# Kernel tuning notes

Measured on AMD Instinct MI355X. Metric: run time of the kernel, lower is better.

Reference implementation:

```python
import jax, jax.numpy as jnp
import numpy as np

K_NB = 16
HID = 64
CIN = 128
EPS = 1e-5


def knn_idx(q, t, k):
    # q [B,N,3] queries, t [B,M,3] targets -> idx [B,N,k] into targets
    d = (jnp.sum(q * q, -1)[:, :, None] + jnp.sum(t * t, -1)[:, None, :]
         - 2.0 * jnp.einsum('bnd,bmd->bnm', q, t))
    _, idx = jax.lax.top_k(-d, k)
    return idx


def gather(feat, idx):
    # feat [B,C,M], idx [B,N,K] -> [B,C,N,K]
    return jax.vmap(lambda f, i: f[:, i])(feat, idx)


def conv1x1(x, W, b):
    # x [B,C,N,K], W [O,C], b [O]
    return jnp.einsum('oc,bcnk->bonk', W, x) + b[None, :, None, None]


def group_norm(x, gamma, beta, groups):
    B, C, N, K = x.shape
    xg = x.reshape(B, groups, C // groups, N, K)
    m = xg.mean(axis=(2, 3, 4), keepdims=True)
    v = xg.var(axis=(2, 3, 4), keepdims=True)
    xg = (xg - m) / jnp.sqrt(v + EPS)
    x = xg.reshape(B, C, N, K)
    return x * gamma[None, :, None, None] + beta[None, :, None, None]


def leaky(x):
    return jnp.where(x >= 0, x, 0.1 * x)


def setup_inputs() -> dict:
    key = jax.random.key(0)
    ks = jax.random.split(key, 20)
    B, N = 2, 4096
    d = {
        'xyz0': jax.random.normal(ks[0], (B, 3, N), jnp.float32),
        'xyz1': jax.random.normal(ks[1], (B, 3, N), jnp.float32),
        'state': jax.random.normal(ks[2], (B, HID, N), jnp.float32),
        'corr0': jax.random.normal(ks[3], (B, HID, N), jnp.float32),
        'feat0': jax.random.normal(ks[4], (B, CIN, N), jnp.float32),
        'feat1': jax.random.normal(ks[5], (B, CIN, N), jnp.float32),
        'flow0': jax.random.normal(ks[6], (B, 3, N), jnp.float32),
        # flow_layer: SetConv(3, [64,64]) -> convs take 3+3=6 then 64 in-chans
        'fw1': jax.random.normal(ks[7], (64, 6), jnp.float32) * 0.05,
        'fb1': jnp.zeros((64,), jnp.float32),
        'fg1': jnp.ones((64,), jnp.float32),
        'fbe1': jnp.zeros((64,), jnp.float32),
        'fw2': jax.random.normal(ks[8], (64, 64), jnp.float32) * 0.05,
        'fb2': jnp.zeros((64,), jnp.float32),
        'fg2': jnp.ones((64,), jnp.float32),
        'fbe2': jnp.zeros((64,), jnp.float32),
        # GRU gates: SetConv in_feat = hid(64)+(hid+64=128)=192, +3 = 195 -> 64, no act
        'wz': jax.random.normal(ks[9], (HID, 195), jnp.float32) * 0.05,
        'bz': jnp.zeros((HID,), jnp.float32),
        'wr': jax.random.normal(ks[10], (HID, 195), jnp.float32) * 0.05,
        'br': jnp.zeros((HID,), jnp.float32),
        'wq': jax.random.normal(ks[11], (HID, 195), jnp.float32) * 0.05,
        'bq': jnp.zeros((HID,), jnp.float32),
        # interp weight_net: 2*128+3=259 -> 128 -> 64
        'wa1': jax.random.normal(ks[12], (CIN, 2 * CIN + 3), jnp.float32) * 0.05,
        'ba1': jnp.zeros((CIN,), jnp.float32),
        'wa2': jax.random.normal(ks[13], (HID, CIN), jnp.float32) * 0.05,
        'ba2': jnp.zeros((HID,), jnp.float32),
    }
    return d


def reference(xyz0, xyz1, state, corr0, feat0, feat1, flow0,
              fw1, fb1, fg1, fbe1, fw2, fb2, fg2, fbe2,
              wz, bz, wr, br, wq, bq, wa1, ba1, wa2, ba2):
    xyz0_t = xyz0.transpose(0, 2, 1)  # [B,N,3]
    xyz1_t = xyz1.transpose(0, 2, 1)

    # ---- flow_layer: SetConv (KNN, N==npoint so new_xyz = xyz0) ----
    idx0 = knn_idx(xyz0_t, xyz0_t, K_NB)              # [B,N,K]
    gxyz0 = gather(xyz0, idx0) - xyz0[:, :, :, None]  # [B,3,N,K]
    h = jnp.concatenate([gather(flow0, idx0), gxyz0], axis=1)  # [B,6,N,K]
    h = leaky(group_norm(conv1x1(h, fw1, fb1), fg1, fbe1, 64 // 16))
    h = leaky(group_norm(conv1x1(h, fw2, fb2), fg2, fbe2, 64 // 16))
    flow_feat = h.max(axis=3)  # [B,64,N]

    # ---- iter_layer: SetGRU over xyz0 neighbors ----
    feat_g = jnp.concatenate([corr0, flow_feat], axis=1)  # [B,128,N]

    def gate(f, W, b):
        g = jnp.concatenate([gather(f, idx0), gxyz0], axis=1)
        return conv1x1(g, W, b).max(axis=3)  # [B,64,N]

    hid_in = jnp.concatenate([feat_g, state], axis=1)  # [B,192,N]
    z = jax.nn.sigmoid(gate(hid_in, wz, bz))
    r = jax.nn.sigmoid(gate(hid_in, wr, br))
    q = jnp.tanh(gate(jnp.concatenate([feat_g, r * state], axis=1), wq, bq))
    next_state = (1.0 - z) * state + z * q  # [B,64,N]

    # ---- align_layer: SetInterp (queries xyz1, targets xyz0) ----
    idx1 = knn_idx(xyz1_t, xyz0_t, K_NB)
    gv = gather(next_state, idx1)                        # [B,64,N,K]
    gx = gather(xyz0, idx1) - xyz1[:, :, :, None]        # [B,3,N,K]
    gf = jnp.concatenate([
        gather(feat0, idx1),
        jnp.broadcast_to(feat1[:, :, :, None], feat1.shape + (K_NB,))], axis=1)
    w = conv1x1(jnp.concatenate([gf, gx], axis=1), wa1, ba1)
    w = conv1x1(leaky(w), wa2, ba2)
    w = jax.nn.softmax(w, axis=3)
    return jnp.sum(gv * w, axis=3)  # [B,64,N]
```

## Files before the change

kernel.cpp:

```cpp
#include <hip/hip_runtime.h>

#define B_SZ 2

__device__ __forceinline__ int rfl(int x) { return __builtin_amdgcn_readfirstlane(x); }
__device__ __forceinline__ float leaky(float v) { return v >= 0.f ? v : 0.1f * v; }

__launch_bounds__(256)
__global__ void pack_kernel(const float* __restrict__ xyz, float4* __restrict__ out, int N)
{
  int b = blockIdx.y;
  int i = blockIdx.x * 256 + threadIdx.x;
  if (i >= N) return;
  const float* p = xyz + (size_t)b * 3 * N;
  float x = p[i], y = p[N + i], z = p[2 * N + i];
  out[(size_t)b * N + i] = make_float4(x, y, z, x * x + y * y + z * z);
}

__launch_bounds__(256)
__global__ void knn_wave_kernel(const float4* __restrict__ pk, const float* __restrict__ q,
                                int* __restrict__ idx, int N)
{
  __shared__ float sx[1024], sy[1024], sz[1024], sw[1024];
  int b = blockIdx.y;
  int lane = threadIdx.x & 63, wav = rfl(threadIdx.x >> 6);
  int qi = blockIdx.x * 4 + wav;
  const float* qb = q + (size_t)b * 3 * N;
  float qx = qb[qi], qy = qb[N + qi], qz = qb[2 * N + qi];
  float qq = qx * qx + qy * qy + qz * qz;
  float bd = 3.0e38f;
  int   bi = 0;
  float thr = 3.0e38f;
  const float4* pb = pk + (size_t)b * N;
  for (int ch = 0; ch < N; ch += 1024) {
    __syncthreads();
    for (int i = threadIdx.x; i < 1024; i += 256) {
      float4 v = pb[ch + i];
      sx[i] = v.x; sy[i] = v.y; sz[i] = v.z; sw[i] = v.w;
    }
    __syncthreads();
    for (int sub = 0; sub < 1024; sub += 64) {
      int c = sub + lane;
      float dl = (qq + sw[c]) - 2.0f * (qx * sx[c] + qy * sy[c] + qz * sz[c]);
      unsigned long long qm = __ballot(dl < thr);
      while (qm) {
        int l = __ffsll(qm) - 1;
        qm &= qm - 1;
        float dc = __shfl(dl, l);
        unsigned long long rm = __ballot(lane < 16 && bd <= dc);
        int pos = __popcll(rm);
        if (pos < 16) {
          int ic = ch + sub + l;
          float pbd = __shfl(bd, lane - 1);
          int   pbi = __shfl(bi, lane - 1);
          if (lane < 16) {
            if (lane == pos)      { bd = dc;  bi = ic; }
            else if (lane > pos)  { bd = pbd; bi = pbi; }
          }
          thr = __shfl(bd, 15);
        }
      }
    }
  }
  if (lane < 16) idx[((size_t)b * N + qi) * 16 + lane] = bi;
}

__launch_bounds__(256)
__global__ void prep_w_kernel(const float* __restrict__ wz, const float* __restrict__ wr,
    const float* __restrict__ wq, const float* __restrict__ wa1,
    const float* __restrict__ bz, const float* __restrict__ br,
    float* __restrict__ WtZR, float* __restrict__ WtQ,
    float* __restrict__ WtU, float* __restrict__ WtV, float* __restrict__ bZR)
{
  int job = blockIdx.x;
  int tid = threadIdx.x;
  if (job == 0) {
    for (int e = tid; e < 195 * 128; e += 256) {
      int k = e >> 7, o = e & 127;
      const float* w = (o < 64) ? wz : wr;
      WtZR[(size_t)k * 128 + o] = w[(size_t)(o & 63) * 195 + k];
    }
    if (tid < 128) bZR[tid] = (tid < 64) ? bz[tid] : br[tid - 64];
  } else if (job == 1) {
    for (int e = tid; e < 195 * 64; e += 256) {
      int k = e >> 6, o = e & 63;
      WtQ[(size_t)k * 64 + o] = wq[(size_t)o * 195 + k];
    }
  } else if (job == 2) {
    for (int e = tid; e < 131 * 128; e += 256) {
      int k = e >> 7, o = e & 127;
      int col = (k < 128) ? k : 256 + (k - 128);
      WtU[(size_t)k * 128 + o] = wa1[(size_t)o * 259 + col];
    }
  } else {
    for (int e = tid; e < 131 * 128; e += 256) {
      int k = e >> 7, o = e & 127;
      float v = (k < 128) ? wa1[(size_t)o * 259 + 128 + k]
                          : -wa1[(size_t)o * 259 + 256 + (k - 128)];
      WtV[(size_t)k * 128 + o] = v;
    }
  }
}

#define KC 66
__launch_bounds__(256)
__global__ void projT_kernel(const float* __restrict__ Wt, int K, int WOUT,
    const float* __restrict__ bias, float* __restrict__ out,
    int N, int PN,
    const float* __restrict__ s0, int c0, int l0,
    const float* __restrict__ s1, int c1, int l1,
    const float* __restrict__ s2, int c2, int l2,
    const float* __restrict__ s3, int c3, int l3)
{
  __shared__ __align__(16) float Ws[KC][68];
  __shared__ __align__(16) float Xs[KC][68];
  const int n0 = blockIdx.x * 64;
  const int oo = blockIdx.y * 64;
  const int b = n0 / N;
  const int nn0 = n0 - b * N;
  const int tid = threadIdx.x;
  const int tx = tid & 15, ty = tid >> 4;
  const int o4 = tx * 4, n4 = ty * 4;
  float acc[4][4];
#pragma unroll
  for (int i = 0; i < 4; ++i)
#pragma unroll
    for (int j = 0; j < 4; ++j)
      acc[i][j] = bias ? bias[oo + o4 + j] : 0.0f;

  const int e01 = c0 + c1, e012 = c0 + c1 + c2;
  for (int k0 = 0; k0 < K; k0 += KC) {
    const int kc = min(KC, K - k0);
    __syncthreads();
    for (int e = tid; e < kc * 64; e += 256) {
      int k = e >> 6, o = e & 63;
      Ws[k][o] = Wt[(size_t)(k0 + k) * WOUT + oo + o];
    }
    for (int e = tid; e < kc * 64; e += 256) {
      int k = e >> 6, j = e & 63;
      int c = k0 + k;
      float v;
      if (c < c0)        v = l0 ? s0[(size_t)c * PN + n0 + j]
                                : s0[((size_t)b * c0 + c) * N + nn0 + j];
      else if (c < e01)  { int cc = c - c0;
                           v = l1 ? s1[(size_t)cc * PN + n0 + j]
                                  : s1[((size_t)b * c1 + cc) * N + nn0 + j]; }
      else if (c < e012) { int cc = c - e01;
                           v = l2 ? s2[(size_t)cc * PN + n0 + j]
                                  : s2[((size_t)b * c2 + cc) * N + nn0 + j]; }
      else               { int cc = c - e012;
                           v = l3 ? s3[(size_t)cc * PN + n0 + j]
                                  : s3[((size_t)b * c3 + cc) * N + nn0 + j]; }
      Xs[k][j] = v;
    }
    __syncthreads();
#pragma unroll 2
    for (int k = 0; k < kc; ++k) {
      float4 wv = *(const float4*)&Ws[k][o4];
      float4 xv = *(const float4*)&Xs[k][n4];
      acc[0][0] = fmaf(xv.x, wv.x, acc[0][0]); acc[0][1] = fmaf(xv.x, wv.y, acc[0][1]);
      acc[0][2] = fmaf(xv.x, wv.z, acc[0][2]); acc[0][3] = fmaf(xv.x, wv.w, acc[0][3]);
      acc[1][0] = fmaf(xv.y, wv.x, acc[1][0]); acc[1][1] = fmaf(xv.y, wv.y, acc[1][1]);
      acc[1][2] = fmaf(xv.y, wv.z, acc[1][2]); acc[1][3] = fmaf(xv.y, wv.w, acc[1][3]);
      acc[2][0] = fmaf(xv.z, wv.x, acc[2][0]); acc[2][1] = fmaf(xv.z, wv.y, acc[2][1]);
      acc[2][2] = fmaf(xv.z, wv.z, acc[2][2]); acc[2][3] = fmaf(xv.z, wv.w, acc[2][3]);
      acc[3][0] = fmaf(xv.w, wv.x, acc[3][0]); acc[3][1] = fmaf(xv.w, wv.y, acc[3][1]);
      acc[3][2] = fmaf(xv.w, wv.z, acc[3][2]); acc[3][3] = fmaf(xv.w, wv.w, acc[3][3]);
    }
  }
#pragma unroll
  for (int i = 0; i < 4; ++i) {
    float4 r = make_float4(acc[i][0], acc[i][1], acc[i][2], acc[i][3]);
    *(float4*)&out[(size_t)(n0 + n4 + i) * WOUT + oo + o4] = r;
  }
}

__device__ __forceinline__ void seg_accumL(const float* __restrict__ p, int cnt,
    const float* __restrict__ WL, int sC, int sN, long n0, float acc[4])
{
#pragma unroll 4
  for (int c = 0; c < cnt; ++c) {
    float w = WL[c];
    const float* pp = p + (size_t)c * sC + (size_t)n0 * sN;
#pragma unroll
    for (int m = 0; m < 4; ++m)
      acc[m] = fmaf(w, pp[(size_t)m * sN], acc[m]);
  }
}

template<int WP>
__launch_bounds__(256)
__global__ void proj_kernel(
    const float* __restrict__ W0, const float* __restrict__ bias,
    float* __restrict__ out, int OUTS, int wld, int N,
    const float* __restrict__ s0, int c0, int w0,
    const float* __restrict__ s1, int c1, int w1)
{
  __shared__ float Wl[64 * WP];
  const int b = blockIdx.y;
  const int lane = threadIdx.x & 63;
  const int wav = rfl(threadIdx.x >> 6);
  int lco = 0;
  for (int r = wav; r < 64; r += 4)
    for (int c = lane; c < c0; c += 64)
      Wl[r * WP + c] = W0[(size_t)r * wld + w0 + c];
  lco = c0;
  for (int r = wav; r < 64; r += 4)
    for (int c = lane; c < c1; c += 64)
      Wl[r * WP + lco + c] = W0[(size_t)r * wld + w1 + c];
  __syncthreads();
  const long n0 = ((long)blockIdx.x * 4 + wav) * 4;
  float bv = bias ? bias[lane] : 0.0f;
  float acc[4] = {bv, bv, bv, bv};
  const float* WL = &Wl[lane * WP];
  seg_accumL(s0 + (size_t)b * c0 * N, c0, WL, N, 1, n0, acc);
  seg_accumL(s1 + (size_t)b * c1 * N, c1, WL + c0, N, 1, n0, acc);
#pragma unroll
  for (int m = 0; m < 4; ++m)
    out[((size_t)b * N + n0 + m) * OUTS + lane] = acc[m];
}

__launch_bounds__(256)
__global__ void gn1_stats_kernel(const float* __restrict__ G1, const float* __restrict__ xyz0,
    const float* __restrict__ fw1, const int* __restrict__ idx0,
    float* __restrict__ stats1, int N)
{
  __shared__ float red[4][4][2];
  int b = blockIdx.y;
  int lane = threadIdx.x & 63, wav = rfl(threadIdx.x >> 6);
  float wg0 = fw1[lane * 6 + 3], wg1 = fw1[lane * 6 + 4], wg2 = fw1[lane * 6 + 5];
  const float* xb = xyz0 + (size_t)b * 3 * N;
  float sum = 0.f, sq = 0.f;
  for (int n = blockIdx.x * 4 + wav; n < N; n += gridDim.x * 4) {
    const int* ip = idx0 + ((size_t)b * N + n) * 16;
    float bx = wg0 * xb[n] + wg1 * xb[N + n] + wg2 * xb[2 * N + n];
#pragma unroll
    for (int k = 0; k < 16; ++k) {
      int m = ip[k];
      float y = G1[((size_t)b * N + m) * 64 + lane] - bx;
      sum += y; sq += y * y;
    }
  }
#pragma unroll
  for (int off = 1; off < 16; off <<= 1) {
    sum += __shfl_xor(sum, off, 64);
    sq += __shfl_xor(sq, off, 64);
  }
  int g = lane >> 4;
  if ((lane & 15) == 0) { red[wav][g][0] = sum; red[wav][g][1] = sq; }
  __syncthreads();
  if (threadIdx.x < 8) {
    int gg = threadIdx.x >> 1, s = threadIdx.x & 1;
    float v = red[0][gg][s] + red[1][gg][s] + red[2][gg][s] + red[3][gg][s];
    atomicAdd(&stats1[(b * 4 + gg) * 2 + s], v);
  }
}

__global__ void gn_finalize_kernel(const float* __restrict__ raw, float* __restrict__ mi, float cnt)
{
  int i = threadIdx.x;
  if (i < 8) {
    float s = raw[i * 2], q = raw[i * 2 + 1];
    float m = s / cnt;
    float v = q / cnt - m * m;
    mi[i * 2] = m;
    mi[i * 2 + 1] = rsqrtf(v + 1e-5f);
  }
}

__launch_bounds__(256, 2)
__global__ void conv2_kernel(const float* __restrict__ G1, const float* __restrict__ xyz0,
    const float* __restrict__ fw1, const int* __restrict__ idx0,
    const float* __restrict__ fw2, const float* __restrict__ fb2,
    const float* __restrict__ fg1, const float* __restrict__ fbe1,
    const float* __restrict__ mi1, float* __restrict__ y2max, float* __restrict__ y2min,
    float* __restrict__ stats2, int N)
{
  __shared__ __align__(16) float x2[4][16][64];
  __shared__ float red[4][4][2];
  const int b = blockIdx.y;
  const int lane = threadIdx.x & 63;
  const int wav = rfl(threadIdx.x >> 6);
  float4 w[16];
#pragma unroll
  for (int i = 0; i < 16; ++i) w[i] = *(const float4*)&fw2[lane * 64 + i * 4];
  float wg0 = fw1[lane * 6 + 3], wg1 = fw1[lane * 6 + 4], wg2 = fw1[lane * 6 + 5];
  const int g = lane >> 4;
  float mu1 = mi1[(b * 4 + g) * 2], inv1 = mi1[(b * 4 + g) * 2 + 1];
  float sc1 = fg1[lane] * inv1;
  float sh1 = fbe1[lane] - mu1 * sc1;
  float fb2l = fb2[lane];
  const float* xb = xyz0 + (size_t)b * 3 * N;
  float sum = 0.f, sq = 0.f;
  for (int n = blockIdx.x * 4 + wav; n < N; n += gridDim.x * 4) {
    const int* ip = idx0 + ((size_t)b * N + n) * 16;
    float bx = wg0 * xb[n] + wg1 * xb[N + n] + wg2 * xb[2 * N + n];
#pragma unroll
    for (int k = 0; k < 16; ++k) {
      int m = ip[k];
      float y = G1[((size_t)b * N + m) * 64 + lane] - bx;
      x2[wav][k][lane] = leaky(y * sc1 + sh1);
    }
    float acc[16];
#pragma unroll
    for (int k = 0; k < 16; ++k) acc[k] = fb2l;
#pragma unroll
    for (int c4 = 0; c4 < 16; ++c4) {
      float4 w4 = w[c4];
#pragma unroll
      for (int k = 0; k < 16; ++k) {
        float4 x4 = *(const float4*)&x2[wav][k][c4 * 4];
        acc[k] = fmaf(w4.x, x4.x, acc[k]);
        acc[k] = fmaf(w4.y, x4.y, acc[k]);
        acc[k] = fmaf(w4.z, x4.z, acc[k]);
        acc[k] = fmaf(w4.w, x4.w, acc[k]);
      }
    }
    float mx = -3.0e38f, mn = 3.0e38f;
#pragma unroll
    for (int k = 0; k < 16; ++k) {
      mx = fmaxf(mx, acc[k]); mn = fminf(mn, acc[k]);
      sum += acc[k]; sq += acc[k] * acc[k];
    }
    y2max[((size_t)b * N + n) * 64 + lane] = mx;
    y2min[((size_t)b * N + n) * 64 + lane] = mn;
  }
#pragma unroll
  for (int off = 1; off < 16; off <<= 1) {
    sum += __shfl_xor(sum, off, 64);
    sq += __shfl_xor(sq, off, 64);
  }
  if ((lane & 15) == 0) { red[wav][g][0] = sum; red[wav][g][1] = sq; }
  __syncthreads();
  if (threadIdx.x < 8) {
    int gg = threadIdx.x >> 1, s = threadIdx.x & 1;
    float v = red[0][gg][s] + red[1][gg][s] + red[2][gg][s] + red[3][gg][s];
    atomicAdd(&stats2[(b * 4 + gg) * 2 + s], v);
  }
}

__launch_bounds__(256)
__global__ void flow_feat_kernel(const float* __restrict__ y2max, const float* __restrict__ y2min,
    const float* __restrict__ mi2, const float* __restrict__ fg2, const float* __restrict__ fbe2,
    float* __restrict__ ff_t, int N, int PN)
{
  size_t i = (size_t)blockIdx.x * blockDim.x + threadIdx.x;
  if (i >= (size_t)B_SZ * N * 64) return;
  int c = i & 63;
  size_t pn = i >> 6;
  int b = (int)(pn / N);
  int g = c >> 4;
  float mu = mi2[(b * 4 + g) * 2], inv = mi2[(b * 4 + g) * 2 + 1];
  float sc = fg2[c] * inv;
  float sh = fbe2[c] - mu * sc;
  float y = (sc >= 0.0f) ? y2max[i] : y2min[i];
  ff_t[(size_t)c * PN + pn] = leaky(y * sc + sh);
}

__launch_bounds__(256)
__global__ void gate_zr_kernel(const float* __restrict__ Szr,
    const float* __restrict__ wz, const float* __restrict__ wr,
    const float* __restrict__ xyz0, const float* __restrict__ state,
    const int* __restrict__ idx0,
    float* __restrict__ zo, float* __restrict__ rs_t, int N, int PN)
{
  int b = blockIdx.y;
  int lane = threadIdx.x & 63, wav = rfl(threadIdx.x >> 6);
  float wz0 = wz[lane * 195 + 192], wz1 = wz[lane * 195 + 193], wz2 = wz[lane * 195 + 194];
  float wr0 = wr[lane * 195 + 192], wr1 = wr[lane * 195 + 193], wr2 = wr[lane * 195 + 194];
  const float* xb = xyz0 + (size_t)b * 3 * N;
  for (int n = blockIdx.x * 4 + wav; n < N; n += gridDim.x * 4) {
    const int* ip = idx0 + ((size_t)b * N + n) * 16;
    float u0 = xb[n], u1 = xb[N + n], u2 = xb[2 * N + n];
    float xz = wz0 * u0 + wz1 * u1 + wz2 * u2;
    float xr = wr0 * u0 + wr1 * u1 + wr2 * u2;
    float mz = -3.0e38f, mr = -3.0e38f;
#pragma unroll
    for (int k = 0; k < 16; ++k) {
      size_t mo = ((size_t)b * N + ip[k]) * 128 + lane;
      mz = fmaxf(mz, Szr[mo]);
      mr = fmaxf(mr, Szr[mo + 64]);
    }
    size_t no = ((size_t)b * N + n) * 64 + lane;
    float z = 1.f / (1.f + expf(-(mz - xz)));
    float r = 1.f / (1.f + expf(-(mr - xr)));
    zo[no] = z;
    rs_t[(size_t)lane * PN + (size_t)b * N + n] = r * state[((size_t)b * 64 + lane) * N + n];
  }
}

__launch_bounds__(256)
__global__ void gate_q_ns_kernel(const float* __restrict__ Sq, const float* __restrict__ wq,
    const float* __restrict__ xyz0, const float* __restrict__ zo,
    const float* __restrict__ state, const int* __restrict__ idx0,
    float* __restrict__ ns, int N)
{
  int b = blockIdx.y;
  int lane = threadIdx.x & 63, wav = rfl(threadIdx.x >> 6);
  float wq0 = wq[lane * 195 + 192], wq1 = wq[lane * 195 + 193], wq2 = wq[lane * 195 + 194];
  const float* xb = xyz0 + (size_t)b * 3 * N;
  for (int n = blockIdx.x * 4 + wav; n < N; n += gridDim.x * 4) {
    const int* ip = idx0 + ((size_t)b * N + n) * 16;
    float xq = wq0 * xb[n] + wq1 * xb[N + n] + wq2 * xb[2 * N + n];
    float mq = -3.0e38f;
#pragma unroll
    for (int k = 0; k < 16; ++k)
      mq = fmaxf(mq, Sq[((size_t)b * N + ip[k]) * 64 + lane]);
    size_t no = ((size_t)b * N + n) * 64 + lane;
    float q = tanhf(mq - xq);
    float z = zo[no];
    float st = state[((size_t)b * 64 + lane) * N + n];
    ns[no] = (1.f - z) * st + z * q;
  }
}

__launch_bounds__(256, 2)
__global__ void align_kernel(const float* __restrict__ U, const float* __restrict__ V,
    const float* __restrict__ wa2, const float* __restrict__ ba2,
    const float* __restrict__ ns, const int* __restrict__ idx1,
    float* __restrict__ out, int N)
{
  __shared__ __align__(16) float xk[4][16][128];
  const int b = blockIdx.y;
  const int lane = threadIdx.x & 63;
  const int wav = rfl(threadIdx.x >> 6);
  float4 w[32];
#pragma unroll
  for (int i = 0; i < 32; ++i) w[i] = *(const float4*)&wa2[lane * 128 + i * 4];
  float ba = ba2[lane];
  const int n = blockIdx.x * 4 + wav;
  const int* ip = idx1 + ((size_t)b * N + n) * 16;
  int mk[16];
#pragma unroll
  for (int k = 0; k < 16; ++k) mk[k] = ip[k];
  const float* Vp = V + ((size_t)b * N + n) * 128;
  float v0 = Vp[lane], v1 = Vp[64 + lane];
#pragma unroll
  for (int k = 0; k < 16; ++k) {
    const float* Up = U + ((size_t)b * N + mk[k]) * 128;
    xk[wav][k][lane] = leaky(Up[lane] + v0);
    xk[wav][k][64 + lane] = leaky(Up[64 + lane] + v1);
  }
  float acc[16];
#pragma unroll
  for (int k = 0; k < 16; ++k) acc[k] = ba;
#pragma unroll
  for (int c4 = 0; c4 < 32; ++c4) {
    float4 w4 = w[c4];
#pragma unroll
    for (int k = 0; k < 16; ++k) {
      float4 x4 = *(const float4*)&xk[wav][k][c4 * 4];
      acc[k] = fmaf(w4.x, x4.x, acc[k]);
      acc[k] = fmaf(w4.y, x4.y, acc[k]);
      acc[k] = fmaf(w4.z, x4.z, acc[k]);
      acc[k] = fmaf(w4.w, x4.w, acc[k]);
    }
  }
  float m = acc[0];
#pragma unroll
  for (int k = 1; k < 16; ++k) m = fmaxf(m, acc[k]);
  float s = 0.f;
#pragma unroll
  for (int k = 0; k < 16; ++k) { acc[k] = expf(acc[k] - m); s += acc[k]; }
  float rinv = 1.0f / s;
  float o = 0.f;
#pragma unroll
  for (int k = 0; k < 16; ++k)
    o += acc[k] * rinv * ns[((size_t)b * N + mk[k]) * 64 + lane];
  out[((size_t)b * 64 + lane) * N + n] = o;
}

extern "C" void kernel_launch(void* const* d_in, const int* in_sizes, int n_in,
                              void* d_out, int out_size, void* d_ws, size_t ws_size,
                              hipStream_t stream) {
  (void)n_in; (void)out_size; (void)ws_size;
  const float* xyz0 = (const float*)d_in[0];
  const float* xyz1 = (const float*)d_in[1];
  const float* state = (const float*)d_in[2];
  const float* corr0 = (const float*)d_in[3];
  const float* feat0 = (const float*)d_in[4];
  const float* feat1 = (const float*)d_in[5];
  const float* flow0 = (const float*)d_in[6];
  const float* fw1 = (const float*)d_in[7];
  const float* fb1 = (const float*)d_in[8];
  const float* fg1 = (const float*)d_in[9];
  const float* fbe1 = (const float*)d_in[10];
  const float* fw2 = (const float*)d_in[11];
  const float* fb2 = (const float*)d_in[12];
  const float* fg2 = (const float*)d_in[13];
  const float* fbe2 = (const float*)d_in[14];
  const float* wz = (const float*)d_in[15];
  const float* bz = (const float*)d_in[16];
  const float* wr = (const float*)d_in[17];
  const float* br = (const float*)d_in[18];
  const float* wq = (const float*)d_in[19];
  const float* bq = (const float*)d_in[20];
  const float* wa1 = (const float*)d_in[21];
  const float* ba1 = (const float*)d_in[22];
  const float* wa2 = (const float*)d_in[23];
  const float* ba2 = (const float*)d_in[24];
  float* out = (float*)d_out;

  const int N = in_sizes[0] / (3 * B_SZ);
  const int PN = B_SZ * N;
  char* wsb = (char*)d_ws;
  size_t off = 0;
  auto take = [&](size_t bytes) -> char* {
    char* p = wsb + off;
    off += (bytes + 255) & ~(size_t)255;
    return p;
  };
  float* U    = (float*)take((size_t)PN * 128 * 4);
  float* V    = (float*)take((size_t)PN * 128 * 4);
  float* Szr  = (float*)take((size_t)PN * 128 * 4);
  float4* pk0 = (float4*)take((size_t)PN * 4 * 4);
  int*   idx0 = (int*)  take((size_t)PN * 16 * 4);
  int*   idx1 = (int*)  take((size_t)PN * 16 * 4);
  float* G1   = (float*)take((size_t)PN * 64 * 4);
  float* y2mx = (float*)take((size_t)PN * 64 * 4);
  float* y2mn = (float*)take((size_t)PN * 64 * 4);
  float* ff_t = (float*)take((size_t)PN * 64 * 4);
  float* Sq   = (float*)take((size_t)PN * 64 * 4);
  float* zg   = (float*)take((size_t)PN * 64 * 4);
  float* rs_t = (float*)take((size_t)PN * 64 * 4);
  float* ns   = (float*)take((size_t)PN * 64 * 4);
  float* WtZR = (float*)take(195 * 128 * 4);
  float* WtQ  = (float*)take(195 * 64 * 4);
  float* WtU  = (float*)take(131 * 128 * 4);
  float* WtV  = (float*)take(131 * 128 * 4);
  float* bZR  = (float*)take(128 * 4);
  float* stats = (float*)take(256);
  float* raw1 = stats, *raw2 = stats + 16, *mi1 = stats + 32, *mi2 = stats + 48;

  const float* FN = nullptr;
  const float cntv = 16.0f * N * 16.0f;

  hipMemsetAsync(raw1, 0, 32 * sizeof(float), stream);

  pack_kernel<<<dim3((N + 255) / 256, B_SZ), 256, 0, stream>>>(xyz0, pk0, N);
  prep_w_kernel<<<4, 256, 0, stream>>>(wz, wr, wq, wa1, bz, br, WtZR, WtQ, WtU, WtV, bZR);
  knn_wave_kernel<<<dim3(N / 4, B_SZ), 256, 0, stream>>>(pk0, xyz0, idx0, N);
  knn_wave_kernel<<<dim3(N / 4, B_SZ), 256, 0, stream>>>(pk0, xyz1, idx1, N);

  proj_kernel<7><<<dim3(N / 16, B_SZ), 256, 0, stream>>>(
      fw1, fb1, G1, 64, 6, N, flow0, 3, 0, xyz0, 3, 3);

  gn1_stats_kernel<<<dim3(256, B_SZ), 256, 0, stream>>>(G1, xyz0, fw1, idx0, raw1, N);
  gn_finalize_kernel<<<1, 64, 0, stream>>>(raw1, mi1, cntv);
  conv2_kernel<<<dim3(512, B_SZ), 256, 0, stream>>>(G1, xyz0, fw1, idx0, fw2, fb2, fg1, fbe1,
      mi1, y2mx, y2mn, raw2, N);
  gn_finalize_kernel<<<1, 64, 0, stream>>>(raw2, mi2, cntv);
  flow_feat_kernel<<<dim3((unsigned)((size_t)PN * 64 / 256)), 256, 0, stream>>>(
      y2mx, y2mn, mi2, fg2, fbe2, ff_t, N, PN);

  projT_kernel<<<dim3(PN / 64, 2), 256, 0, stream>>>(WtZR, 195, 128, bZR, Szr, N, PN,
      corr0, 64, 0,  ff_t, 64, 1,  state, 64, 0,  xyz0, 3, 0);

  gate_zr_kernel<<<dim3(256, B_SZ), 256, 0, stream>>>(Szr, wz, wr, xyz0, state, idx0, zg, rs_t, N, PN);

  projT_kernel<<<dim3(PN / 64, 1), 256, 0, stream>>>(WtQ, 195, 64, bq, Sq, N, PN,
      corr0, 64, 0,  ff_t, 64, 1,  rs_t, 64, 1,  xyz0, 3, 0);

  gate_q_ns_kernel<<<dim3(256, B_SZ), 256, 0, stream>>>(Sq, wq, xyz0, zg, state, idx0, ns, N);

  projT_kernel<<<dim3(PN / 64, 2), 256, 0, stream>>>(WtU, 131, 128, FN, U, N, PN,
      feat0, 128, 0,  xyz0, 3, 0,  FN, 0, 0,  FN, 0, 0);
  projT_kernel<<<dim3(PN / 64, 2), 256, 0, stream>>>(WtV, 131, 128, ba1, V, N, PN,
      feat1, 128, 0,  xyz1, 3, 0,  FN, 0, 0,  FN, 0, 0);

  align_kernel<<<dim3(N / 4, B_SZ), 256, 0, stream>>>(U, V, wa2, ba2, ns, idx1, out, N);
}
```

Baseline: 408.1 us.

## Replace serial KNN insertion with threshold-filter plus bitonic sort selection

The KNN kernel now makes two passes. The first computes per-lane minimum distances and takes a threshold that guarantees at least 16 candidates. The second compacts candidates under that threshold into shared memory and picks the top 16 with a wave-level bitonic sort. This replaces the serialized ballot/shuffle insertion loop and is meant to cut divergent per-candidate work, at the cost of reading the target points twice. Candidates are capped at 256, which could drop true neighbors if that many tie under the threshold.

```diff
diff --git a/kernel.cpp b/kernel.cpp
--- a/kernel.cpp
+++ b/kernel.cpp
@@ -16,52 +16,95 @@
   out[(size_t)b * N + i] = make_float4(x, y, z, x * x + y * y + z * z);
 }
 
+__device__ __forceinline__ void sort64(float& d, int& i, int lane)
+{
+#pragma unroll
+  for (int k = 2; k <= 64; k <<= 1) {
+#pragma unroll
+    for (int j = k >> 1; j > 0; j >>= 1) {
+      float od = __shfl_xor(d, j, 64);
+      int   oi = __shfl_xor(i, j, 64);
+      bool mineSmall = (d < od) || (d == od && i < oi);
+      bool amLow = (lane & j) == 0;
+      bool up = (lane & k) == 0;
+      bool keepMine = (amLow == up) ? mineSmall : !mineSmall;
+      if (!keepMine) { d = od; i = oi; }
+    }
+  }
+}
+
 __launch_bounds__(256)
 __global__ void knn_wave_kernel(const float4* __restrict__ pk, const float* __restrict__ q,
                                 int* __restrict__ idx, int N)
 {
-  __shared__ float sx[1024], sy[1024], sz[1024], sw[1024];
-  int b = blockIdx.y;
-  int lane = threadIdx.x & 63, wav = rfl(threadIdx.x >> 6);
-  int qi = blockIdx.x * 4 + wav;
+  __shared__ __align__(16) float4 ts[1024];
+  __shared__ uint2 buf[4][256];
+  const int b = blockIdx.y;
+  const int lane = threadIdx.x & 63, wav = rfl(threadIdx.x >> 6);
+  const int qi = blockIdx.x * 4 + wav;
   const float* qb = q + (size_t)b * 3 * N;
-  float qx = qb[qi], qy = qb[N + qi], qz = qb[2 * N + qi];
-  float qq = qx * qx + qy * qy + qz * qz;
-  float bd = 3.0e38f;
-  int   bi = 0;
-  float thr = 3.0e38f;
+  const float qx = qb[qi], qy = qb[N + qi], qz = qb[2 * N + qi];
+  const float qq = qx * qx + qy * qy + qz * qz;
   const float4* pb = pk + (size_t)b * N;
+
+  float lmin = 3.0e38f;
   for (int ch = 0; ch < N; ch += 1024) {
     __syncthreads();
-    for (int i = threadIdx.x; i < 1024; i += 256) {
-      float4 v = pb[ch + i];
-      sx[i] = v.x; sy[i] = v.y; sz[i] = v.z; sw[i] = v.w;
-    }
+    for (int i = threadIdx.x; i < 1024; i += 256) ts[i] = pb[ch + i];
     __syncthreads();
-    for (int sub = 0; sub < 1024; sub += 64) {
-      int c = sub + lane;
-      float dl = (qq + sw[c]) - 2.0f * (qx * sx[c] + qy * sy[c] + qz * sz[c]);
-      unsigned long long qm = __ballot(dl < thr);
-      while (qm) {
-        int l = __ffsll(qm) - 1;
-        qm &= qm - 1;
-        float dc = __shfl(dl, l);
-        unsigned long long rm = __ballot(lane < 16 && bd <= dc);
-        int pos = __popcll(rm);
-        if (pos < 16) {
-          int ic = ch + sub + l;
-          float pbd = __shfl(bd, lane - 1);
-          int   pbi = __shfl(bi, lane - 1);
-          if (lane < 16) {
-            if (lane == pos)      { bd = dc;  bi = ic; }
-            else if (lane > pos)  { bd = pbd; bi = pbi; }
-          }
-          thr = __shfl(bd, 15);
+#pragma unroll 4
+    for (int sub = 0; sub < 16; ++sub) {
+      float4 v = ts[sub * 64 + lane];
+      float key = (qq + v.w) - 2.0f * (qx * v.x + qy * v.y + qz * v.z);
+      lmin = fminf(lmin, key);
+    }
+  }
+  float gm = fminf(lmin, __shfl_xor(lmin, 1, 64));
+  gm = fminf(gm, __shfl_xor(gm, 2, 64));
+  float t0 = gm;
+  t0 = fmaxf(t0, __shfl_xor(t0, 4, 64));
+  t0 = fmaxf(t0, __shfl_xor(t0, 8, 64));
+  t0 = fmaxf(t0, __shfl_xor(t0, 16, 64));
+  t0 = fmaxf(t0, __shfl_xor(t0, 32, 64));
+
+  int cnt = 0;
+  for (int ch = 0; ch < N; ch += 1024) {
+    __syncthreads();
+    for (int i = threadIdx.x; i < 1024; i += 256) ts[i] = pb[ch + i];
+    __syncthreads();
+    for (int sub = 0; sub < 16; ++sub) {
+      float4 v = ts[sub * 64 + lane];
+      float key = (qq + v.w) - 2.0f * (qx * v.x + qy * v.y + qz * v.z);
+      bool qf = key <= t0;
+      unsigned long long mask = __ballot(qf);
+      if (mask) {
+        unsigned lo = __builtin_amdgcn_mbcnt_lo((unsigned)mask, 0u);
+        unsigned pre = __builtin_amdgcn_mbcnt_hi((unsigned)(mask >> 32), lo);
+        if (qf) {
+          unsigned slot = (unsigned)cnt + pre;
+          if (slot < 256u)
+            buf[wav][slot] = make_uint2(__float_as_uint(key), (unsigned)(ch + sub * 64 + lane));
         }
+        cnt += (int)__popcll(mask);
       }
     }
   }
-  if (lane < 16) idx[((size_t)b * N + qi) * 16 + lane] = bi;
+  int C = cnt < 256 ? cnt : 256;
+
+  float kd = 3.0e38f; int ki = 0x7fffffff;
+  if (lane < C) { uint2 u = buf[wav][lane]; kd = __uint_as_float(u.x); ki = (int)u.y; }
+  sort64(kd, ki, lane);
+  int consumed = C < 64 ? C : 64;
+  while (consumed < C) {
+    if (lane >= 16) {
+      int j2 = consumed + (lane - 16);
+      if (j2 < C) { uint2 u = buf[wav][j2]; kd = __uint_as_float(u.x); ki = (int)u.y; }
+      else { kd = 3.0e38f; ki = 0x7fffffff; }
+    }
+    int t = C - consumed; consumed += (t < 48 ? t : 48);
+    sort64(kd, ki, lane);
+  }
+  if (lane < 16) idx[((size_t)b * N + qi) * 16 + lane] = ki;
 }
 
 __launch_bounds__(256)
@@ -199,14 +242,12 @@
   const int b = blockIdx.y;
   const int lane = threadIdx.x & 63;
   const int wav = rfl(threadIdx.x >> 6);
-  int lco = 0;
   for (int r = wav; r < 64; r += 4)
     for (int c = lane; c < c0; c += 64)
       Wl[r * WP + c] = W0[(size_t)r * wld + w0 + c];
-  lco = c0;
   for (int r = wav; r < 64; r += 4)
     for (int c = lane; c < c1; c += 64)
-      Wl[r * WP + lco + c] = W0[(size_t)r * wld + w1 + c];
+      Wl[r * WP + c0 + c] = W0[(size_t)r * wld + w1 + c];
   __syncthreads();
   const long n0 = ((long)blockIdx.x * 4 + wav) * 4;
   float bv = bias ? bias[lane] : 0.0f;
```

New measurement: 368.2 us. 9.8% less time.
